# Kernel optimization log

Hardware: AMD Instinct MI355X
Metric: run time of the kernel (lower is better)

Reference implementation:

```python
import jax, jax.numpy as jnp
import numpy as np

B, P, D, E, H = 8, 512, 16, 64, 128

# fixed fully-connected (no self-loop) edge list
_mask = ~np.eye(P, dtype=bool)
_S_IDX, _R_IDX = np.nonzero(_mask)  # senders, receivers; Ne = P*(P-1)
S_IDX = jnp.asarray(_S_IDX, dtype=jnp.int32)
R_IDX = jnp.asarray(_R_IDX, dtype=jnp.int32)


def setup_inputs() -> dict:
    key = jax.random.key(0)
    ks = jax.random.split(key, 6)
    def lin(k, fan_in, shape):
        return jax.random.normal(k, shape, jnp.float32) / jnp.sqrt(jnp.float32(fan_in))
    return {
        "h": jax.random.normal(ks[0], (B, P * D), jnp.float32),
        "We1": lin(ks[1], 2 * D + 1, (2 * D + 1, H)),
        "be1": jnp.zeros((H,), jnp.float32),
        "We2": lin(ks[2], H, (H, E)),
        "be2": jnp.zeros((E,), jnp.float32),
        "Wn1": lin(ks[3], E + D, (E + D, H)),
        "bn1": jnp.zeros((H,), jnp.float32),
        "Wn2": lin(ks[4], H, (H, D)),
        "bn2": jnp.zeros((D,), jnp.float32),
        "t": 0,
    }


def reference(h, We1, be1, We2, be2, Wn1, bn1, Wn2, bn2, t):
    nodes = h.reshape(-1, P, D)                      # [B, P, D]
    ns = nodes[:, S_IDX, :]                          # gather senders  [B, Ne, D]
    nr = nodes[:, R_IDX, :]                          # gather receivers [B, Ne, D]
    dist = jnp.linalg.norm(ns - nr, axis=-1, keepdims=True)  # [B, Ne, 1]
    # EdgeBlock: concat(edge_attr, receiver, sender) -> MLP
    e_in = jnp.concatenate([dist, nr, ns], axis=-1)  # [B, Ne, 2D+1]
    e = jax.nn.relu(e_in @ We1 + be1) @ We2 + be2    # [B, Ne, E]
    # NodeBlock: scatter-sum received edges per node, concat with node feats
    agg = jnp.zeros((nodes.shape[0], P, E), e.dtype).at[:, R_IDX, :].add(e)
    n_in = jnp.concatenate([agg, nodes], axis=-1)    # [B, P, E+D]
    new_nodes = jax.nn.relu(n_in @ Wn1 + bn1) @ Wn2 + bn2  # [B, P, D]
    return new_nodes.reshape(-1, P * D)
```

## Files before the change

kernel.cpp:

```cpp
#include <hip/hip_runtime.h>


#define Bc 8
#define Pc 512
#define Dc 16
#define Ec 64
#define Hc 128
#define RT 4

__global__ __launch_bounds__(256) void gin_precompute_G(
    const float* __restrict__ hIn, const float* __restrict__ We1, float* __restrict__ G) {
  const int node = blockIdx.x * 2 + (threadIdx.x >> 7);
  const int j = threadIdx.x & (Hc - 1);
  const float* n = hIn + node * Dc;
  float acc = 0.f;
#pragma unroll
  for (int k = 0; k < Dc; ++k) acc = fmaf(n[k], We1[(17 + k) * Hc + j], acc);
  G[node * Hc + j] = acc;
}

__global__ __launch_bounds__(256) void gin_main(
    const float* __restrict__ hIn, const float* __restrict__ We1, const float* __restrict__ be1,
    const float* __restrict__ We2, const float* __restrict__ be2,
    const float* __restrict__ Wn1, const float* __restrict__ bn1,
    const float* __restrict__ Wn2, const float* __restrict__ bn2,
    const float* __restrict__ G, float* __restrict__ out) {
  const int tid  = threadIdx.x;
  const int j    = tid & (Hc - 1);
  const int half = tid >> 7;
  const int blk  = blockIdx.x;
  const int b    = blk / (Pc / RT);
  const int rb   = blk % (Pc / RT);
  const int r0   = rb * RT;

  const float* nodes = hIn + b * Pc * Dc;
  const float* Gb    = G + b * Pc * Hc;

  __shared__ float s_dist[RT][Pc];
  __shared__ float s_nr[RT][Dc];
  __shared__ float s_hsum[RT][Hc];
  __shared__ float s_nin[RT][Ec + Dc];
  __shared__ float s_h2[RT][Hc];

  if (tid < RT * Dc) {
    int k = tid / Dc, d = tid % Dc;
    s_nr[k][d] = nodes[(r0 + k) * Dc + d];
  }
  __syncthreads();

  for (int idx = tid; idx < RT * Pc; idx += 256) {
    int k = idx / Pc, s = idx % Pc;
    const float* ns = nodes + s * Dc;
    float acc = 0.f;
#pragma unroll
    for (int d = 0; d < Dc; ++d) {
      float df = ns[d] - s_nr[k][d];
      acc = fmaf(df, df, acc);
    }
    s_dist[k][s] = sqrtf(acc);
  }

  const float w0 = We1[j];
  float br[RT];
#pragma unroll
  for (int k = 0; k < RT; ++k) {
    float acc = be1[j];
#pragma unroll
    for (int d = 0; d < Dc; ++d) acc = fmaf(s_nr[k][d], We1[(1 + d) * Hc + j], acc);
    br[k] = acc;
  }
  __syncthreads();

  float acc0 = 0.f, acc1 = 0.f, acc2 = 0.f, acc3 = 0.f;
  const int s_begin = half * (Pc / 2);
#pragma unroll 4
  for (int s = s_begin; s < s_begin + Pc / 2; ++s) {
    float g = Gb[s * Hc + j];
    acc0 += fmaxf(fmaf(s_dist[0][s], w0, g + br[0]), 0.f);
    acc1 += fmaxf(fmaf(s_dist[1][s], w0, g + br[1]), 0.f);
    acc2 += fmaxf(fmaf(s_dist[2][s], w0, g + br[2]), 0.f);
    acc3 += fmaxf(fmaf(s_dist[3][s], w0, g + br[3]), 0.f);
  }

  if (half == 1) {
    s_hsum[0][j] = acc0; s_hsum[1][j] = acc1; s_hsum[2][j] = acc2; s_hsum[3][j] = acc3;
  }
  __syncthreads();
  if (half == 0) {
    float a[RT] = {acc0, acc1, acc2, acc3};
#pragma unroll
    for (int k = 0; k < RT; ++k) {
      float corr = fmaxf(Gb[(r0 + k) * Hc + j] + br[k], 0.f);
      s_hsum[k][j] += a[k] - corr;
    }
  }
  __syncthreads();

  {
    int k = tid >> 6, e = tid & (Ec - 1);
    float acc = 511.0f * be2[e];
#pragma unroll 16
    for (int jj = 0; jj < Hc; ++jj) acc = fmaf(s_hsum[k][jj], We2[jj * Ec + e], acc);
    s_nin[k][e] = acc;
  }
  if (tid < RT * Dc) {
    int k = tid / Dc, d = tid % Dc;
    s_nin[k][Ec + d] = s_nr[k][d];
  }
  __syncthreads();

#pragma unroll
  for (int kk = 0; kk < RT / 2; ++kk) {
    int k = half * (RT / 2) + kk;
    float acc = bn1[j];
#pragma unroll 16
    for (int i = 0; i < Ec + Dc; ++i) acc = fmaf(s_nin[k][i], Wn1[i * Hc + j], acc);
    s_h2[k][j] = fmaxf(acc, 0.f);
  }
  __syncthreads();

  if (tid < RT * Dc) {
    int k = tid >> 4, d = tid & (Dc - 1);
    float acc = bn2[d];
#pragma unroll 16
    for (int jj = 0; jj < Hc; ++jj) acc = fmaf(s_h2[k][jj], Wn2[jj * Dc + d], acc);
    out[b * Pc * Dc + (r0 + k) * Dc + d] = acc;
  }
}

extern "C" void kernel_launch(void* const* d_in, const int* in_sizes, int n_in,
                              void* d_out, int out_size, void* d_ws, size_t ws_size,
                              hipStream_t stream) {
  const float* h   = (const float*)d_in[0];
  const float* We1 = (const float*)d_in[1];
  const float* be1 = (const float*)d_in[2];
  const float* We2 = (const float*)d_in[3];
  const float* be2 = (const float*)d_in[4];
  const float* Wn1 = (const float*)d_in[5];
  const float* bn1 = (const float*)d_in[6];
  const float* Wn2 = (const float*)d_in[7];
  const float* bn2 = (const float*)d_in[8];
  float* out = (float*)d_out;
  float* G   = (float*)d_ws;

  gin_precompute_G<<<Bc * Pc / 2, 256, 0, stream>>>(h, We1, G);
  gin_main<<<Bc * Pc / RT, 256, 0, stream>>>(h, We1, be1, We2, be2, Wn1, bn1, Wn2, bn2, G, out);
}
```

Baseline: 120.9 us.

## Pack hidden pairs into float2 and split sender loop four ways with packed math

G is now stored interleaved as float2 pairs (j, j+64), and each thread processes two hidden units using 2-wide vector FMA/max intended to map to packed fp32 instructions. The sender loop is split across four 64-thread quarters with shared-memory partial reduction. Distances are computed with float4 loads and stored as float4 per sender. The precompute kernel stages weights and nodes in shared memory. This aims to halve instruction count in the hot loop, at the cost of an extra reduction stage and more shared memory.

Measured after the change: 126.6 us. +4.7%, slower.

```diff
diff --git a/kernel.cpp b/kernel.cpp
--- a/kernel.cpp
+++ b/kernel.cpp
@@ -7,16 +7,46 @@
 #define Ec 64
 #define Hc 128
 #define RT 4
+#define NB 16
+
+typedef float v2f __attribute__((ext_vector_type(2)));
+
+__device__ __forceinline__ v2f v2fma(v2f a, v2f b, v2f c) {
+#if __has_builtin(__builtin_elementwise_fma)
+  return __builtin_elementwise_fma(a, b, c);
+#else
+  v2f r; r.x = fmaf(a.x, b.x, c.x); r.y = fmaf(a.y, b.y, c.y); return r;
+#endif
+}
+__device__ __forceinline__ v2f v2max0(v2f a) {
+  v2f z = {0.f, 0.f};
+#if __has_builtin(__builtin_elementwise_max)
+  return __builtin_elementwise_max(a, z);
+#else
+  v2f r; r.x = fmaxf(a.x, 0.f); r.y = fmaxf(a.y, 0.f); return r;
+#endif
+}
 
 __global__ __launch_bounds__(256) void gin_precompute_G(
-    const float* __restrict__ hIn, const float* __restrict__ We1, float* __restrict__ G) {
-  const int node = blockIdx.x * 2 + (threadIdx.x >> 7);
-  const int j = threadIdx.x & (Hc - 1);
-  const float* n = hIn + node * Dc;
-  float acc = 0.f;
+    const float* __restrict__ hIn, const float* __restrict__ We1, float2* __restrict__ Gp) {
+  __shared__ float sW[Dc][Hc];
+  __shared__ float sN[NB][Dc];
+  const int tid = threadIdx.x;
+  for (int i = tid; i < Dc * Hc; i += 256) sW[i >> 7][i & 127] = We1[17 * Hc + i];
+  const int base = blockIdx.x * NB;
+  for (int i = tid; i < NB * Dc; i += 256) sN[i >> 4][i & 15] = hIn[base * Dc + i];
+  __syncthreads();
+  for (int idx = tid; idx < NB * 64; idx += 256) {
+    int node = idx >> 6, j2 = idx & 63;
+    float a0 = 0.f, a1 = 0.f;
 #pragma unroll
-  for (int k = 0; k < Dc; ++k) acc = fmaf(n[k], We1[(17 + k) * Hc + j], acc);
-  G[node * Hc + j] = acc;
+    for (int d = 0; d < Dc; ++d) {
+      float nv = sN[node][d];
+      a0 = fmaf(nv, sW[d][j2], a0);
+      a1 = fmaf(nv, sW[d][j2 + 64], a1);
+    }
+    Gp[(base + node) * 64 + j2] = make_float2(a0, a1);
+  }
 }
 
 __global__ __launch_bounds__(256) void gin_main(
@@ -24,107 +54,128 @@
     const float* __restrict__ We2, const float* __restrict__ be2,
     const float* __restrict__ Wn1, const float* __restrict__ bn1,
     const float* __restrict__ Wn2, const float* __restrict__ bn2,
-    const float* __restrict__ G, float* __restrict__ out) {
-  const int tid  = threadIdx.x;
-  const int j    = tid & (Hc - 1);
-  const int half = tid >> 7;
-  const int blk  = blockIdx.x;
-  const int b    = blk / (Pc / RT);
-  const int rb   = blk % (Pc / RT);
-  const int r0   = rb * RT;
+    const float2* __restrict__ Gp, float* __restrict__ out) {
+  const int tid = threadIdx.x;
+  const int q   = tid >> 6;
+  const int j2  = tid & 63;
+  const int blk = blockIdx.x;
+  const int b   = blk >> 7;
+  const int rb  = blk & 127;
+  const int r0  = rb * RT;
 
-  const float* nodes = hIn + b * Pc * Dc;
-  const float* Gb    = G + b * Pc * Hc;
+  const float*  nodes = hIn + b * Pc * Dc;
+  const float2* Gb    = Gp + (size_t)b * Pc * 64;
 
-  __shared__ float s_dist[RT][Pc];
-  __shared__ float s_nr[RT][Dc];
-  __shared__ float s_hsum[RT][Hc];
-  __shared__ float s_nin[RT][Ec + Dc];
-  __shared__ float s_h2[RT][Hc];
+  __shared__ float4 s_dist4[Pc];
+  __shared__ float  s_nr[RT][Dc];
+  __shared__ v2f    s_part[4][RT][64];
+  __shared__ float  s_hsum[RT][Hc];
+  __shared__ float  s_nin[RT][Ec + Dc];
+  __shared__ float  s_h2[RT][Hc];
 
-  if (tid < RT * Dc) {
-    int k = tid / Dc, d = tid % Dc;
-    s_nr[k][d] = nodes[(r0 + k) * Dc + d];
-  }
+  if (tid < RT * Dc) s_nr[tid >> 4][tid & 15] = nodes[r0 * Dc + tid];
   __syncthreads();
 
-  for (int idx = tid; idx < RT * Pc; idx += 256) {
-    int k = idx / Pc, s = idx % Pc;
-    const float* ns = nodes + s * Dc;
-    float acc = 0.f;
+#pragma unroll
+  for (int it = 0; it < 2; ++it) {
+    int s = tid + it * 256;
+    const float4* ns4 = (const float4*)(nodes + s * Dc);
+    float nsv[Dc];
+    *(float4*)(nsv + 0)  = ns4[0];
+    *(float4*)(nsv + 4)  = ns4[1];
+    *(float4*)(nsv + 8)  = ns4[2];
+    *(float4*)(nsv + 12) = ns4[3];
+    float dk[RT];
+#pragma unroll
+    for (int k = 0; k < RT; ++k) {
+      float acc = 0.f;
+#pragma unroll
+      for (int d = 0; d < Dc; ++d) {
+        float df = nsv[d] - s_nr[k][d];
+        acc = fmaf(df, df, acc);
+      }
+      dk[k] = sqrtf(acc);
+    }
+    s_dist4[s] = make_float4(dk[0], dk[1], dk[2], dk[3]);
+  }
+
+  v2f w02 = {We1[j2], We1[j2 + 64]};
+  v2f br2[RT];
+  {
+    v2f be = {be1[j2], be1[j2 + 64]};
+#pragma unroll
+    for (int k = 0; k < RT; ++k) br2[k] = be;
 #pragma unroll
     for (int d = 0; d < Dc; ++d) {
-      float df = ns[d] - s_nr[k][d];
-      acc = fmaf(df, df, acc);
-    }
-    s_dist[k][s] = sqrtf(acc);
-  }
-
-  const float w0 = We1[j];
-  float br[RT];
+      v2f wrow = {We1[(1 + d) * Hc + j2], We1[(1 + d) * Hc + j2 + 64]};
 #pragma unroll
-  for (int k = 0; k < RT; ++k) {
-    float acc = be1[j];
-#pragma unroll
-    for (int d = 0; d < Dc; ++d) acc = fmaf(s_nr[k][d], We1[(1 + d) * Hc + j], acc);
-    br[k] = acc;
-  }
-  __syncthreads();
-
-  float acc0 = 0.f, acc1 = 0.f, acc2 = 0.f, acc3 = 0.f;
-  const int s_begin = half * (Pc / 2);
-#pragma unroll 4
-  for (int s = s_begin; s < s_begin + Pc / 2; ++s) {
-    float g = Gb[s * Hc + j];
-    acc0 += fmaxf(fmaf(s_dist[0][s], w0, g + br[0]), 0.f);
-    acc1 += fmaxf(fmaf(s_dist[1][s], w0, g + br[1]), 0.f);
-    acc2 += fmaxf(fmaf(s_dist[2][s], w0, g + br[2]), 0.f);
-    acc3 += fmaxf(fmaf(s_dist[3][s], w0, g + br[3]), 0.f);
-  }
-
-  if (half == 1) {
-    s_hsum[0][j] = acc0; s_hsum[1][j] = acc1; s_hsum[2][j] = acc2; s_hsum[3][j] = acc3;
-  }
-  __syncthreads();
-  if (half == 0) {
-    float a[RT] = {acc0, acc1, acc2, acc3};
-#pragma unroll
-    for (int k = 0; k < RT; ++k) {
-      float corr = fmaxf(Gb[(r0 + k) * Hc + j] + br[k], 0.f);
-      s_hsum[k][j] += a[k] - corr;
+      for (int k = 0; k < RT; ++k) {
+        v2f nv = {s_nr[k][d], s_nr[k][d]};
+        br2[k] = v2fma(nv, wrow, br2[k]);
+      }
     }
   }
   __syncthreads();
 
+  v2f acc[RT] = {};
+  const float2* gq = Gb + (size_t)(q * 128) * 64 + j2;
+  const float4* dq = s_dist4 + q * 128;
+#pragma unroll 4
+  for (int s = 0; s < 128; ++s) {
+    float4 d4 = dq[s];
+    float2 gg = gq[(size_t)s * 64];
+    v2f g = {gg.x, gg.y};
+    v2f dd, t;
+    dd = (v2f){d4.x, d4.x}; t = v2fma(dd, w02, g + br2[0]); acc[0] += v2max0(t);
+    dd = (v2f){d4.y, d4.y}; t = v2fma(dd, w02, g + br2[1]); acc[1] += v2max0(t);
+    dd = (v2f){d4.z, d4.z}; t = v2fma(dd, w02, g + br2[2]); acc[2] += v2max0(t);
+    dd = (v2f){d4.w, d4.w}; t = v2fma(dd, w02, g + br2[3]); acc[3] += v2max0(t);
+  }
+#pragma unroll
+  for (int k = 0; k < RT; ++k) s_part[q][k][j2] = acc[k];
+  __syncthreads();
+
   {
-    int k = tid >> 6, e = tid & (Ec - 1);
-    float acc = 511.0f * be2[e];
-#pragma unroll 16
-    for (int jj = 0; jj < Hc; ++jj) acc = fmaf(s_hsum[k][jj], We2[jj * Ec + e], acc);
-    s_nin[k][e] = acc;
-  }
-  if (tid < RT * Dc) {
-    int k = tid / Dc, d = tid % Dc;
-    s_nin[k][Ec + d] = s_nr[k][d];
+    int k = q;
+    v2f sum = s_part[0][k][j2] + s_part[1][k][j2] + s_part[2][k][j2] + s_part[3][k][j2];
+    float2 gg = Gb[(size_t)(r0 + k) * 64 + j2];
+    v2f gs = {gg.x, gg.y};
+    sum -= v2max0(gs + br2[k]);
+    s_hsum[k][j2]      = sum.x;
+    s_hsum[k][j2 + 64] = sum.y;
   }
   __syncthreads();
 
+  {
+    int k = tid >> 6, e = tid & 63;
+    float a = 511.0f * be2[e];
+#pragma unroll 16
+    for (int jj = 0; jj < Hc; ++jj) a = fmaf(s_hsum[k][jj], We2[jj * Ec + e], a);
+    s_nin[k][e] = a;
+  }
+  if (tid < RT * Dc) s_nin[tid >> 4][Ec + (tid & 15)] = s_nr[tid >> 4][tid & 15];
+  __syncthreads();
+
+  {
+    const int j = tid & 127;
+    const int half = tid >> 7;
 #pragma unroll
-  for (int kk = 0; kk < RT / 2; ++kk) {
-    int k = half * (RT / 2) + kk;
-    float acc = bn1[j];
+    for (int kk = 0; kk < 2; ++kk) {
+      int k = half * 2 + kk;
+      float a = bn1[j];
 #pragma unroll 16
-    for (int i = 0; i < Ec + Dc; ++i) acc = fmaf(s_nin[k][i], Wn1[i * Hc + j], acc);
-    s_h2[k][j] = fmaxf(acc, 0.f);
+      for (int i = 0; i < Ec + Dc; ++i) a = fmaf(s_nin[k][i], Wn1[i * Hc + j], a);
+      s_h2[k][j] = fmaxf(a, 0.f);
+    }
   }
   __syncthreads();
 
   if (tid < RT * Dc) {
-    int k = tid >> 4, d = tid & (Dc - 1);
-    float acc = bn2[d];
+    int k = tid >> 4, d = tid & 15;
+    float a = bn2[d];
 #pragma unroll 16
-    for (int jj = 0; jj < Hc; ++jj) acc = fmaf(s_h2[k][jj], Wn2[jj * Dc + d], acc);
-    out[b * Pc * Dc + (r0 + k) * Dc + d] = acc;
+    for (int jj = 0; jj < Hc; ++jj) a = fmaf(s_h2[k][jj], Wn2[jj * Dc + d], a);
+    out[b * Pc * Dc + (r0 + k) * Dc + d] = a;
   }
 }
 
@@ -141,8 +192,8 @@
   const float* Wn2 = (const float*)d_in[7];
   const float* bn2 = (const float*)d_in[8];
   float* out = (float*)d_out;
-  float* G   = (float*)d_ws;
+  float2* Gp = (float2*)d_ws;
 
-  gin_precompute_G<<<Bc * Pc / 2, 256, 0, stream>>>(h, We1, G);
-  gin_main<<<Bc * Pc / RT, 256, 0, stream>>>(h, We1, be1, We2, be2, Wn1, bn1, Wn2, bn2, G, out);
+  gin_precompute_G<<<(Bc * Pc) / NB, 256, 0, stream>>>(h, We1, Gp);
+  gin_main<<<Bc * (Pc / RT), 256, 0, stream>>>(h, We1, be1, We2, be2, Wn1, bn1, Wn2, bn2, Gp, out);
 }
```
